# Kernel tuning notes

Measured on AMD Instinct MI355X. Metric: run time of the kernel, lower is better.

## Reference

```python
import jax, jax.numpy as jnp
import numpy as np

B, T, F = 256, 512, 64      # batch, input_win, feature_m
U1, U2, OUT = 256, 128, 24  # GRU1 units, GRU2 units, output_win


def _gru_seq(x, K, R, b):
    """Keras GRU (reset_after=True, tanh/sigmoid). x: [B,T,F] -> [B,T,U].
    K: [F,3U] input kernel, R: [U,3U] recurrent kernel, b: [2,3U] (input bias, recurrent bias).
    Gate order: z (update), r (reset), h (candidate).
    """
    u = R.shape[0]
    # Precompute all input projections in one big GEMM: [B,T,3U]
    xg = jnp.einsum('btf,fg->btg', x, K) + b[0]

    def step(h, xt):
        rg = h @ R + b[1]                       # [B,3U] recurrent projection
        xz, xr, xh = jnp.split(xt, 3, axis=-1)
        rz, rr, rh = jnp.split(rg, 3, axis=-1)
        z = jax.nn.sigmoid(xz + rz)
        r = jax.nn.sigmoid(xr + rr)
        hh = jnp.tanh(xh + r * rh)              # reset_after: r applied after matmul
        hn = z * h + (1.0 - z) * hh
        return hn, hn

    h0 = jnp.zeros((x.shape[0], u), x.dtype)
    _, hs = jax.lax.scan(step, h0, jnp.swapaxes(xg, 0, 1))  # scan over time
    return jnp.swapaxes(hs, 0, 1)  # [B,T,U]


def setup_inputs() -> dict:
    key = jax.random.key(0)
    ks = jax.random.split(key, 12)
    s = lambda k, shape: jax.random.normal(k, shape, jnp.float32) * 0.05
    return {
        'x':  jax.random.normal(ks[0], (B, T, F), jnp.float32),
        'k1': s(ks[1], (F, 3 * U1)),
        'r1': s(ks[2], (U1, 3 * U1)),
        'b1': jnp.zeros((2, 3 * U1), jnp.float32),
        'k2': s(ks[3], (U1, 3 * U2)),
        'r2': s(ks[4], (U2, 3 * U2)),
        'b2': jnp.zeros((2, 3 * U2), jnp.float32),
        'w3': s(ks[5], (U2, 64)),  'b3': jnp.zeros((64,), jnp.float32),
        'w4': s(ks[6], (64, 32)),  'b4': jnp.zeros((32,), jnp.float32),
        'w5': s(ks[7], (32, OUT)), 'b5': jnp.zeros((OUT,), jnp.float32),
    }


def reference(x, k1, r1, b1, k2, r2, b2, w3, b3, w4, b4, w5, b5):
    h = _gru_seq(x, k1, r1, b1)            # [B,T,256]
    h = _gru_seq(h, k2, r2, b2)[:, -1]     # return_sequences=False -> last state [B,128]
    h = h @ w3 + b3                        # Dense(64), linear activation
    h = h @ w4 + b4                        # Dense(32)
    return h @ w5 + b5                     # Dense(output_win)
```

## Files before the change

### kernel.cpp

```cpp
#include <hip/hip_runtime.h>
#include <hip/hip_fp16.h>
#include <math.h>

#define BATCH 256
#define TSEQ  512
#define FEAT  64
#define NU1   256
#define NU2   128

#define G1Z_OFF 0
#define G1R_OFF 40960
#define G1H_OFF 81920
#define G2Z_OFF 122880
#define G2R_OFF 147456
#define G2H_OFF 172032
#define TOTAL_H2 196608

#define G1Z_U4 0
#define G1R_U4 10240
#define G1H_U4 20480
#define G2Z_U4 30720
#define G2R_U4 36864
#define G2H_U4 43008

#define LDS_PARK_BYTES (9216 * 16)

typedef _Float16 h2f __attribute__((ext_vector_type(2)));

__device__ __forceinline__ float sigmoid_f(float v) {
    return 1.0f / (1.0f + __expf(-v));
}
__device__ __forceinline__ float tanh_f(float v) {
    float c = fminf(fmaxf(v, -15.0f), 15.0f);
    float e = __expf(2.0f * c);
    return (e - 1.0f) / (e + 1.0f);
}

__device__ __forceinline__ h2f bch2(unsigned int u) {
    return __builtin_bit_cast(h2f, u);
}
__device__ __forceinline__ unsigned int pack2(float a, float b) {
    h2f v;
    v.x = (_Float16)a;
    v.y = (_Float16)b;
    return __builtin_bit_cast(unsigned int, v);
}

__device__ __forceinline__ void dot4(float& acc, uint4 w, uint4 a) {
    acc = __builtin_amdgcn_fdot2(bch2(w.x), bch2(a.x), acc, false);
    acc = __builtin_amdgcn_fdot2(bch2(w.y), bch2(a.y), acc, false);
    acc = __builtin_amdgcn_fdot2(bch2(w.z), bch2(a.z), acc, false);
    acc = __builtin_amdgcn_fdot2(bch2(w.w), bch2(a.w), acc, false);
}

__global__ void pack_weights(const float* __restrict__ k1, const float* __restrict__ r1,
                             const float* __restrict__ k2, const float* __restrict__ r2,
                             __half2* __restrict__ ws)
{
    int idx = blockIdx.x * 256 + threadIdx.x;
    if (idx >= TOTAL_H2) return;
    float a, b;
    if (idx < G2Z_OFF) {
        int plane = idx / 40960;
        int rem   = idx % 40960;
        int cc    = rem >> 10;
        int col   = (rem >> 2) & 255;
        int q     = rem & 3;
        int kh    = cc / 20;
        int c     = cc - kh * 20;
        int g     = plane * 256 + col;
        int pair  = (c < 4) ? ((kh * 4 + c) * 4 + q)
                            : (32 + (kh * 16 + (c - 4)) * 4 + q);
        int row0  = pair * 2;
        if (row0 < 64) { a = k1[row0 * 768 + g];        b = k1[(row0 + 1) * 768 + g]; }
        else           { a = r1[(row0 - 64) * 768 + g]; b = r1[(row0 - 63) * 768 + g]; }
    } else {
        int idx2  = idx - G2Z_OFF;
        int plane = idx2 / 24576;
        int rem   = idx2 % 24576;
        int cc    = rem >> 9;
        int col   = (rem >> 2) & 127;
        int q     = rem & 3;
        int kq    = cc / 12;
        int c     = cc - kq * 12;
        int g     = plane * 128 + col;
        int pair  = (c < 8) ? ((kq * 8 + c) * 4 + q)
                            : (128 + (kq * 4 + (c - 8)) * 4 + q);
        int row0  = pair * 2;
        if (row0 < 256) { a = k2[row0 * 384 + g];         b = k2[(row0 + 1) * 384 + g]; }
        else            { a = r2[(row0 - 256) * 384 + g]; b = r2[(row0 - 255) * 384 + g]; }
    }
    __half2 h;
    h.x = __float2half_rn(a);
    h.y = __float2half_rn(b);
    ws[idx] = h;
}

template <int COLS, int NCH>
__device__ __forceinline__ void seg3(const uint4* __restrict__ pz,
                                     const uint4* __restrict__ pr,
                                     const uint4* __restrict__ ph,
                                     const unsigned int* __restrict__ act,
                                     float& az, float& ar, float& a3)
{
    static_assert(NCH % 4 == 0, "NCH must be a multiple of 4");
    uint4 a_z0 = pz[0], a_z1 = pz[COLS];
    uint4 a_r0 = pr[0], a_r1 = pr[COLS];
    uint4 a_h0 = ph[0], a_h1 = ph[COLS];
    #pragma unroll 1
    for (int c = 0; c < NCH; c += 4) {
        const uint4* qz = pz + 2 * COLS;
        const uint4* qr = pr + 2 * COLS;
        const uint4* qh = ph + 2 * COLS;
        uint4 b_z0 = qz[0], b_z1 = qz[COLS];
        uint4 b_r0 = qr[0], b_r1 = qr[COLS];
        uint4 b_h0 = qh[0], b_h1 = qh[COLS];
        const uint4 v0 = *(const uint4*)(act);
        const uint4 v1 = *(const uint4*)(act + 4);
        dot4(az, a_z0, v0); dot4(ar, a_r0, v0); dot4(a3, a_h0, v0);
        dot4(az, a_z1, v1); dot4(ar, a_r1, v1); dot4(a3, a_h1, v1);
        pz += 4 * COLS; pr += 4 * COLS; ph += 4 * COLS;
        if (c + 4 < NCH) {
            a_z0 = pz[0]; a_z1 = pz[COLS];
            a_r0 = pr[0]; a_r1 = pr[COLS];
            a_h0 = ph[0]; a_h1 = ph[COLS];
        }
        const uint4 v2 = *(const uint4*)(act + 8);
        const uint4 v3 = *(const uint4*)(act + 12);
        act += 16;
        dot4(az, b_z0, v2); dot4(ar, b_r0, v2); dot4(a3, b_h0, v2);
        dot4(az, b_z1, v3); dot4(ar, b_r1, v3); dot4(a3, b_h1, v3);
    }
}

template <int COLS>
__device__ __forceinline__ void seg_pair(const uint4* __restrict__ pz,
                                         const uint4* __restrict__ pr,
                                         const uint4* __restrict__ ph,
                                         const unsigned int* __restrict__ act,
                                         float& az, float& ar, float& a3)
{
    uint4 z0 = pz[0], z1 = pz[COLS];
    uint4 r0 = pr[0], r1 = pr[COLS];
    uint4 h0 = ph[0], h1 = ph[COLS];
    const uint4 v0 = *(const uint4*)(act);
    const uint4 v1 = *(const uint4*)(act + 4);
    dot4(az, z0, v0); dot4(ar, r0, v0); dot4(a3, h0, v0);
    dot4(az, z1, v1); dot4(ar, r1, v1); dot4(a3, h1, v1);
}

__global__ __launch_bounds__(512, 2)
void gru_fused(const float* __restrict__ x,
               const float* __restrict__ b1, const float* __restrict__ b2,
               const float* __restrict__ w3, const float* __restrict__ b3,
               const float* __restrict__ w4, const float* __restrict__ b4,
               const float* __restrict__ w5, const float* __restrict__ b5,
               const unsigned int* __restrict__ wp,
               float* __restrict__ out)
{
    extern __shared__ __align__(16) uint4 lwdyn[];
    uint4* lw2 = lwdyn;
    uint4* lw1 = lwdyn + 6144;
    __shared__ __align__(16) unsigned int act1[2][160];
    __shared__ __align__(16) unsigned int act2[2][64];
    __shared__ __align__(16) unsigned int act1s[2][160];
    __shared__ float h2fin[NU2];
    __shared__ float d3[64];
    __shared__ float d4[32];

    const int tid = threadIdx.x;
    const int row = blockIdx.x;
    const int j   = tid >> 1;
    const int kh  = tid & 1;
    const int c2  = tid >> 2;
    const int kq  = tid & 3;

    const uint4* wp4 = (const uint4*)wp;

    for (int i = tid; i < 6144; i += 512) {
        int cg = i >> 9;
        int c  = cg / 3, g = cg - 3 * c;
        lw2[i] = wp4[G2Z_U4 + g * 6144 + (kq * 12 + 8 + c) * 128 + c2];
    }
    for (int i = tid; i < 3072; i += 512) {
        int cg = i >> 9;
        int c  = cg / 3, g = cg - 3 * c;
        lw1[i] = wp4[G1Z_U4 + g * 10240 + (kh * 20 + c) * 256 + j];
    }

    for (int i = tid; i < 2 * 160; i += 512) (&act1[0][0])[i]  = 0u;
    for (int i = tid; i < 2 * 64;  i += 512) (&act2[0][0])[i]  = 0u;
    for (int i = tid; i < 2 * 160; i += 512) (&act1s[0][0])[i] = 0u;

    const float bm1  = (kh == 0) ? 1.0f : 0.0f;
    const float bz1  = (b1[j] + b1[768 + j]) * bm1;
    const float br1  = (b1[256 + j] + b1[1024 + j]) * bm1;
    const float bxh1 = b1[512 + j] * bm1;
    const float brh1 = b1[1280 + j] * bm1;
    const float bm2  = (kq == 0) ? 1.0f : 0.0f;
    const float bz2  = (b2[c2] + b2[384 + c2]) * bm2;
    const float br2  = (b2[128 + c2] + b2[512 + c2]) * bm2;
    const float bxh2 = b2[256 + c2] * bm2;
    const float brh2 = b2[640 + c2] * bm2;

    const uint4* g1z = wp4 + G1Z_U4 + (kh * 20) * 256 + j;
    const uint4* g1r = wp4 + G1R_U4 + (kh * 20) * 256 + j;
    const uint4* g1h = wp4 + G1H_U4 + (kh * 20) * 256 + j;
    const uint4* g2z = wp4 + G2Z_U4 + (kq * 12) * 128 + c2;
    const uint4* g2r = wp4 + G2R_U4 + (kq * 12) * 128 + c2;
    const uint4* g2h = wp4 + G2H_U4 + (kq * 12) * 128 + c2;
    const uint4* l2 = lw2 + tid;
    const uint4* l1 = lw1 + tid;

    __syncthreads();

    if (tid < FEAT) {
        float x0 = x[(size_t)row * TSEQ * FEAT + tid];
        float xb = __shfl_xor(x0, 1);
        if ((tid & 1) == 0) act1[0][tid >> 1] = pack2(x0, xb);
    }
    __syncthreads();

    float hp1 = 0.0f;
    float hp2 = 0.0f;

    for (int t = 0; t < TSEQ; ++t) {
        const int cur = t & 1, nb = cur ^ 1;

        float xpre = 0.0f;
        if (t + 1 < TSEQ && tid < FEAT)
            xpre = x[(size_t)row * TSEQ * FEAT + (t + 1) * FEAT + tid];

        float az = bz1, ar = br1, aA = bxh1, aB = brh1;
        seg_pair<1536>(l1, l1 + 512, l1 + 1024,
                       &act1[cur][kh * 16], az, ar, aA);
        seg_pair<256>(g1z + 2 * 256, g1r + 2 * 256, g1h + 2 * 256,
                      &act1[cur][kh * 16 + 8], az, ar, aA);
        seg3<256, 16>(g1z + 4 * 256, g1r + 4 * 256, g1h + 4 * 256,
                      &act1[cur][32 + kh * 64], az, ar, aB);
        az += __shfl_xor(az, 1);
        ar += __shfl_xor(ar, 1);
        aA += __shfl_xor(aA, 1);
        aB += __shfl_xor(aB, 1);
        {
            const float z  = sigmoid_f(az);
            const float rg = sigmoid_f(ar);
            const float hh = tanh_f(aA + rg * aB);
            const float hn = z * hp1 + (1.0f - z) * hh;
            hp1 = hn;
            const float hnb = __shfl_xor(hn, 2);
            if ((tid & 3) == 0) {
                const unsigned int pk = pack2(hn, hnb);
                const int p = tid >> 2;
                act1[nb][32 + p] = pk;
                act1s[nb][(p >> 5) * 40 + (p & 31)] = pk;
            }
        }
        if (t + 1 < TSEQ && tid < FEAT) {
            float xb = __shfl_xor(xpre, 1);
            if ((tid & 1) == 0) act1[nb][tid >> 1] = pack2(xpre, xb);
        }
        __syncthreads();

        float az2 = bz2, ar2 = br2, aA2 = bxh2, aB2 = brh2;
        seg3<128, 8>(g2z, g2r, g2h, &act1s[nb][kq * 40], az2, ar2, aA2);
        seg3<1536, 4>(l2, l2 + 512, l2 + 1024,
                      &act2[cur][kq * 16], az2, ar2, aB2);
        az2 += __shfl_xor(az2, 1); az2 += __shfl_xor(az2, 2);
        ar2 += __shfl_xor(ar2, 1); ar2 += __shfl_xor(ar2, 2);
        aA2 += __shfl_xor(aA2, 1); aA2 += __shfl_xor(aA2, 2);
        aB2 += __shfl_xor(aB2, 1); aB2 += __shfl_xor(aB2, 2);
        {
            const float z2v = sigmoid_f(az2);
            const float rg2 = sigmoid_f(ar2);
            const float hh2 = tanh_f(aA2 + rg2 * aB2);
            const float hn2 = z2v * hp2 + (1.0f - z2v) * hh2;
            hp2 = hn2;
            const float hnb2 = __shfl_xor(hn2, 4);
            if ((tid & 7) == 0) act2[nb][tid >> 3] = pack2(hn2, hnb2);
        }
    }

    if ((tid & 3) == 0) h2fin[c2] = hp2;
    __syncthreads();

    if (tid < 64) {
        float a = b3[tid];
        #pragma unroll 4
        for (int u = 0; u < NU2; ++u) a += h2fin[u] * w3[u * 64 + tid];
        d3[tid] = a;
    }
    __syncthreads();
    if (tid < 32) {
        float a = b4[tid];
        #pragma unroll 4
        for (int u = 0; u < 64; ++u) a += d3[u] * w4[u * 32 + tid];
        d4[tid] = a;
    }
    __syncthreads();
    if (tid < 24) {
        float a = b5[tid];
        #pragma unroll 4
        for (int u = 0; u < 32; ++u) a += d4[u] * w5[u * 24 + tid];
        out[(size_t)row * 24 + tid] = a;
    }
}

extern "C" void kernel_launch(void* const* d_in, const int* in_sizes, int n_in,
                              void* d_out, int out_size, void* d_ws, size_t ws_size,
                              hipStream_t stream) {
    (void)in_sizes; (void)n_in; (void)ws_size; (void)out_size;
    const float* x  = (const float*)d_in[0];
    const float* k1 = (const float*)d_in[1];
    const float* r1 = (const float*)d_in[2];
    const float* b1 = (const float*)d_in[3];
    const float* k2 = (const float*)d_in[4];
    const float* r2 = (const float*)d_in[5];
    const float* b2 = (const float*)d_in[6];
    const float* w3 = (const float*)d_in[7];
    const float* b3 = (const float*)d_in[8];
    const float* w4 = (const float*)d_in[9];
    const float* b4 = (const float*)d_in[10];
    const float* w5 = (const float*)d_in[11];
    const float* b5 = (const float*)d_in[12];
    float* out = (float*)d_out;

    static bool lds_attr_set = false;
    if (!lds_attr_set) {
        (void)hipFuncSetAttribute((const void*)gru_fused,
                                  hipFuncAttributeMaxDynamicSharedMemorySize,
                                  LDS_PARK_BYTES);
        lds_attr_set = true;
    }

    hipLaunchKernelGGL(pack_weights, dim3((TOTAL_H2 + 255) / 256), dim3(256), 0, stream,
                       k1, r1, k2, r2, (__half2*)d_ws);
    hipLaunchKernelGGL(gru_fused, dim3(BATCH), dim3(512), LDS_PARK_BYTES, stream,
                       x, b1, b2, w3, b3, w4, b4, w5, b5,
                       (const unsigned int*)d_ws, out);
}
```

Baseline: 4.718 ms.

## Stream GRU1 recurrent weights through per-wave LDS ring via async global_load_lds

Replaces the direct global loads of the large GRU1 recurrent-weight segment with a per-wave double-buffered LDS staging ring, filled by global_load_lds and gated by explicit vmcnt waits so the next chunk's fetch overlaps the current dot products. To free LDS for the staging buffers, the GRU2 recurrent weights that used to be parked in LDS are now read from global memory every step. The benefit depends on whether the async prefetch hides latency better than ordinary register loads, against the added global traffic for GRU2. Hand-placed waitcnt and sched_barriers add fragility: if the compiler issues other vector-memory loads in the same window, the vmcnt(6) wait count can be wrong.

```diff
diff --git a/kernel.cpp b/kernel.cpp
--- a/kernel.cpp
+++ b/kernel.cpp
@@ -26,6 +26,10 @@
 #define LDS_PARK_BYTES (9216 * 16)
 
 typedef _Float16 h2f __attribute__((ext_vector_type(2)));
+typedef __attribute__((address_space(3))) void lds_void;
+typedef const __attribute__((address_space(1))) void glob_void;
+#define GLDS16(src, dst) \
+    __builtin_amdgcn_global_load_lds((glob_void*)(src), (lds_void*)(dst), 16, 0, 0)
 
 __device__ __forceinline__ float sigmoid_f(float v) {
     return 1.0f / (1.0f + __expf(-v));
@@ -159,8 +163,8 @@
                float* __restrict__ out)
 {
     extern __shared__ __align__(16) uint4 lwdyn[];
-    uint4* lw2 = lwdyn;
-    uint4* lw1 = lwdyn + 6144;
+    uint4* stg4 = lwdyn;
+    uint4* lw1  = lwdyn + 6144;
     __shared__ __align__(16) unsigned int act1[2][160];
     __shared__ __align__(16) unsigned int act2[2][64];
     __shared__ __align__(16) unsigned int act1s[2][160];
@@ -168,20 +172,39 @@
     __shared__ float d3[64];
     __shared__ float d4[32];
 
-    const int tid = threadIdx.x;
-    const int row = blockIdx.x;
-    const int j   = tid >> 1;
-    const int kh  = tid & 1;
-    const int c2  = tid >> 2;
-    const int kq  = tid & 3;
+    const int tid  = threadIdx.x;
+    const int row  = blockIdx.x;
+    const int j    = tid >> 1;
+    const int kh   = tid & 1;
+    const int c2   = tid >> 2;
+    const int kq   = tid & 3;
+    const int wid  = tid >> 6;
+    const int lane = tid & 63;
 
     const uint4* wp4 = (const uint4*)wp;
-
-    for (int i = tid; i < 6144; i += 512) {
-        int cg = i >> 9;
-        int c  = cg / 3, g = cg - 3 * c;
-        lw2[i] = wp4[G2Z_U4 + g * 6144 + (kq * 12 + 8 + c) * 128 + c2];
-    }
+    const char*  wpb = (const char*)wp;
+
+    const int    cidx = (lane & 1) * 32 + (lane >> 1);
+    const uint4* stgw = stg4 + wid * 768;
+    char*        stgB = (char*)stg4 + wid * 12288;
+    const size_t loff = ((size_t)((lane >> 5) * 20 + 4) * 256 +
+                         (size_t)(wid * 32 + (lane & 31))) * 16;
+    const char* p1zS = wpb + (size_t)G1Z_U4 * 16 + loff;
+    const char* p1rS = wpb + (size_t)G1R_U4 * 16 + loff;
+    const char* p1hS = wpb + (size_t)G1H_U4 * 16 + loff;
+
+    #pragma unroll
+    for (int uu = 0; uu < 2; ++uu) {
+        char* db = stgB + uu * 6144;
+        const size_t c0 = (size_t)(uu * 2) * 4096;
+        GLDS16(p1zS + c0,        db);
+        GLDS16(p1zS + c0 + 4096, db + 1024);
+        GLDS16(p1rS + c0,        db + 2048);
+        GLDS16(p1rS + c0 + 4096, db + 3072);
+        GLDS16(p1hS + c0,        db + 4096);
+        GLDS16(p1hS + c0 + 4096, db + 5120);
+    }
+
     for (int i = tid; i < 3072; i += 512) {
         int cg = i >> 9;
         int c  = cg / 3, g = cg - 3 * c;
@@ -209,7 +232,6 @@
     const uint4* g2z = wp4 + G2Z_U4 + (kq * 12) * 128 + c2;
     const uint4* g2r = wp4 + G2R_U4 + (kq * 12) * 128 + c2;
     const uint4* g2h = wp4 + G2H_U4 + (kq * 12) * 128 + c2;
-    const uint4* l2 = lw2 + tid;
     const uint4* l1 = lw1 + tid;
 
     __syncthreads();
@@ -232,12 +254,35 @@
             xpre = x[(size_t)row * TSEQ * FEAT + (t + 1) * FEAT + tid];
 
         float az = bz1, ar = br1, aA = bxh1, aB = brh1;
-        seg_pair<1536>(l1, l1 + 512, l1 + 1024,
-                       &act1[cur][kh * 16], az, ar, aA);
+        seg_pair<1536>(l1, l1 + 512, l1 + 1024, &act1[cur][kh * 16], az, ar, aA);
         seg_pair<256>(g1z + 2 * 256, g1r + 2 * 256, g1h + 2 * 256,
                       &act1[cur][kh * 16 + 8], az, ar, aA);
-        seg3<256, 16>(g1z + 4 * 256, g1r + 4 * 256, g1h + 4 * 256,
-                      &act1[cur][32 + kh * 64], az, ar, aB);
+        {
+            const unsigned int* ap = &act1[cur][32 + kh * 64];
+            #pragma unroll
+            for (int u = 0; u < 8; ++u) {
+                const int slot = u & 1;
+                asm volatile("s_waitcnt vmcnt(6)" ::: "memory");
+                __builtin_amdgcn_sched_barrier(0);
+                const uint4* sp = stgw + slot * 384;
+                uint4 w0z = sp[cidx],       w0r = sp[128 + cidx], w0h = sp[256 + cidx];
+                uint4 w1z = sp[64 + cidx],  w1r = sp[192 + cidx], w1h = sp[320 + cidx];
+                const uint4 a0 = *(const uint4*)(ap + u * 8);
+                const uint4 a1 = *(const uint4*)(ap + u * 8 + 4);
+                dot4(az, w0z, a0); dot4(ar, w0r, a0); dot4(aB, w0h, a0);
+                dot4(az, w1z, a1); dot4(ar, w1r, a1); dot4(aB, w1h, a1);
+                __builtin_amdgcn_sched_barrier(0);
+                const size_t c0 = (size_t)(((u + 2) & 7) * 2) * 4096;
+                char* db = stgB + slot * 6144;
+                GLDS16(p1zS + c0,        db);
+                GLDS16(p1zS + c0 + 4096, db + 1024);
+                GLDS16(p1rS + c0,        db + 2048);
+                GLDS16(p1rS + c0 + 4096, db + 3072);
+                GLDS16(p1hS + c0,        db + 4096);
+                GLDS16(p1hS + c0 + 4096, db + 5120);
+                __builtin_amdgcn_sched_barrier(0);
+            }
+        }
         az += __shfl_xor(az, 1);
         ar += __shfl_xor(ar, 1);
         aA += __shfl_xor(aA, 1);
@@ -264,8 +309,8 @@
 
         float az2 = bz2, ar2 = br2, aA2 = bxh2, aB2 = brh2;
         seg3<128, 8>(g2z, g2r, g2h, &act1s[nb][kq * 40], az2, ar2, aA2);
-        seg3<1536, 4>(l2, l2 + 512, l2 + 1024,
-                      &act2[cur][kq * 16], az2, ar2, aB2);
+        seg3<128, 4>(g2z + 8 * 128, g2r + 8 * 128, g2h + 8 * 128,
+                     &act2[cur][kq * 16], az2, ar2, aB2);
         az2 += __shfl_xor(az2, 1); az2 += __shfl_xor(az2, 2);
         ar2 += __shfl_xor(ar2, 1); ar2 += __shfl_xor(ar2, 2);
         aA2 += __shfl_xor(aA2, 1); aA2 += __shfl_xor(aA2, 2);
```

Result: slower. 6.319 ms (+33.9%).
